# Kernel tuning notes

Measured on AMD Instinct MI355X. Metric: run time of the kernel, lower is better.

The kernel has to match this reference:

```python
import jax, jax.numpy as jnp
import numpy as np

E = 4
OUT_CH = 32
IN_CH = 32
KSIZE = 3
PAD = 1
TEMPERATURE = 30.0
HIDDEN = IN_CH // 4  # ratio=4


def _dyn_conv(x, w):
    """Per-sample conv. x: [B,C,H,W], w: [B,O,C,k,k] -> [B,O,H,W] (pad=1, stride=1)."""
    def one(xi, wi):
        return jax.lax.conv_general_dilated(
            xi[None], wi, window_strides=(1, 1), padding=[(PAD, PAD), (PAD, PAD)],
            dimension_numbers=('NCHW', 'OIHW', 'NCHW'))[0]
    return jax.vmap(one)(x, w)


def setup_inputs() -> dict:
    key = jax.random.key(0)
    ks = jax.random.split(key, 6)
    x = jax.random.normal(ks[0], (16, IN_CH, 256, 256), dtype=jnp.float32)
    # ControlModule 1x1 convs (bias=False) expressed as matrices
    w_c1 = jax.random.normal(ks[1], (HIDDEN, IN_CH), dtype=jnp.float32) * (2.0 / IN_CH) ** 0.5
    w_c2 = jax.random.normal(ks[2], (E * OUT_CH, HIDDEN), dtype=jnp.float32) * (2.0 / HIDDEN) ** 0.5
    weight1 = jax.random.normal(ks[3], (E, OUT_CH, IN_CH, KSIZE, KSIZE), dtype=jnp.float32)
    weight2 = jax.random.normal(ks[4], (E, OUT_CH, OUT_CH, KSIZE, KSIZE), dtype=jnp.float32)
    weight3 = jax.random.normal(ks[5], (E, OUT_CH, OUT_CH, KSIZE, KSIZE), dtype=jnp.float32)
    return {"x": x, "w_c1": w_c1, "w_c2": w_c2,
            "weight1": weight1, "weight2": weight2, "weight3": weight3}


def reference(x, w_c1, w_c2, weight1, weight2, weight3):
    B = x.shape[0]
    # ControlModule: global average pool -> 1x1 conv -> relu -> 1x1 conv -> softmax over E
    gap = x.mean(axis=(2, 3))                      # [B, C]
    h = jax.nn.relu(gap @ w_c1.T)                  # [B, hidden]
    coeff = (h @ w_c2.T).reshape(B, OUT_CH, E)     # [B, O, E]
    coeff = jax.nn.softmax(coeff / TEMPERATURE, axis=2)

    def assemble(w):  # w: [E, O, C, k, k] -> per-sample [B, O, C, k, k]
        flat = w.reshape(E, OUT_CH, -1)
        agg = jnp.einsum('boe,eoc->boc', coeff, flat)
        return agg.reshape(B, OUT_CH, *w.shape[2:])

    w1 = assemble(weight1)
    w2 = assemble(weight2)
    w3 = assemble(weight3)

    out = _dyn_conv(x, w1)
    out = _dyn_conv(out, w2)
    out = _dyn_conv(out, w3)
    return out
```

## Files before the change

kernel.cpp:

```cpp
#include <hip/hip_runtime.h>

typedef __attribute__((ext_vector_type(8))) short bf16x8;
typedef __attribute__((ext_vector_type(4))) float f32x4;

#define B_   16
#define HW_  256
#define HID_ 8
#define TEMP_ 30.0f

static __device__ inline unsigned short f2bf(float f) {
    unsigned u = __builtin_bit_cast(unsigned, f);
    u = (u + 0x7FFFu + ((u >> 16) & 1u)) >> 16;
    return (unsigned short)u;
}
static __device__ inline unsigned packbf(float a, float b) {
    return (unsigned)f2bf(a) | ((unsigned)f2bf(b) << 16);
}

__global__ __launch_bounds__(256) void gap_kernel(const float* __restrict__ x,
                                                  float* __restrict__ gap) {
    int blk = blockIdx.x;
    int bc = blk >> 2, q = blk & 3;
    const float4* p = (const float4*)(x + ((size_t)bc << 16)) + q * 4096;
    int t = threadIdx.x;
    float s = 0.f;
#pragma unroll
    for (int i = 0; i < 16; ++i) {
        float4 v = p[i * 256 + t];
        s += v.x + v.y + v.z + v.w;
    }
    __shared__ float red[256];
    red[t] = s;
    __syncthreads();
    for (int off = 128; off > 0; off >>= 1) {
        if (t < off) red[t] += red[t + off];
        __syncthreads();
    }
    if (t == 0) atomicAdd(&gap[bc], red[0] * (1.f / 65536.f));
}

__global__ __launch_bounds__(256) void assemble_kernel(
    const float* __restrict__ gap,
    const float* __restrict__ w_c1,
    const float* __restrict__ w_c2,
    const float* __restrict__ wt1,
    const float* __restrict__ wt2,
    const float* __restrict__ wt3,
    unsigned short* __restrict__ wo1,
    unsigned short* __restrict__ wo2,
    unsigned short* __restrict__ wo3)
{
    int b = blockIdx.x;
    int sel = blockIdx.y;
    int t = threadIdx.x;
    __shared__ float gap_s[32], h_s[8], logit_s[128], coeff_s[32][4];
    if (t < 32) gap_s[t] = gap[b * 32 + t];
    __syncthreads();
    if (t < HID_) {
        float a = 0.f;
        for (int c = 0; c < 32; ++c) a += gap_s[c] * w_c1[t * 32 + c];
        h_s[t] = a > 0.f ? a : 0.f;
    }
    __syncthreads();
    if (t < 128) {
        float a = 0.f;
        for (int k = 0; k < HID_; ++k) a += h_s[k] * w_c2[t * HID_ + k];
        logit_s[t] = a * (1.0f / TEMP_);
    }
    __syncthreads();
    if (t < 32) {
        float m = -1e30f;
        for (int e = 0; e < 4; ++e) m = fmaxf(m, logit_s[t * 4 + e]);
        float ex[4], sum = 0.f;
        for (int e = 0; e < 4; ++e) { ex[e] = expf(logit_s[t * 4 + e] - m); sum += ex[e]; }
        for (int e = 0; e < 4; ++e) coeff_s[t][e] = ex[e] / sum;
    }
    __syncthreads();

    const float* wt = sel == 0 ? wt1 : (sel == 1 ? wt2 : wt3);
    unsigned short* wo = sel == 0 ? wo1 : (sel == 1 ? wo2 : wo3);

    for (int idx = t; idx < 9216; idx += 256) {
        int d = idx >> 10;
        int o = (idx >> 5) & 31;
        int c = idx & 31;
        int j = c * 9 + d;
        float v = coeff_s[o][0] * wt[(0 * 32 + o) * 288 + j]
                + coeff_s[o][1] * wt[(1 * 32 + o) * 288 + j]
                + coeff_s[o][2] * wt[(2 * 32 + o) * 288 + j]
                + coeff_s[o][3] * wt[(3 * 32 + o) * 288 + j];
        wo[(size_t)b * 9216 + idx] = f2bf(v);
    }
}

template<int IN_F32, int OUT_F32>
__global__ __launch_bounds__(256) void conv3x3_mfma(
    const void* __restrict__ src,
    const unsigned short* __restrict__ wgt,
    void* __restrict__ dst)
{
    __shared__ uint4 lds[2448];
    int b  = blockIdx.z;
    int x0 = blockIdx.x * 32, y0 = blockIdx.y * 16;
    int t  = threadIdx.x;
    int l15 = t & 15;
    int kg  = (t >> 4) & 3;
    int wv  = t >> 6;

    bf16x8 wf[9][2];
    {
        const uint4* wp = (const uint4*)(wgt + (size_t)b * 9216);
#pragma unroll
        for (int d = 0; d < 9; ++d)
#pragma unroll
            for (int ob = 0; ob < 2; ++ob)
                wf[d][ob] = __builtin_bit_cast(bf16x8, wp[(d * 32 + ob * 16 + l15) * 4 + kg]);
    }

#pragma unroll
    for (int it = 0; it < 10; ++it) {
        int tau = it * 256 + t;
        if (tau < 2448) {
            int px = tau >> 2, cg = tau & 3;
            int yy = px / 34;
            int xx = px - yy * 34;
            int gy = y0 - 1 + yy, gx = x0 - 1 + xx;
            uint4 v = make_uint4(0u, 0u, 0u, 0u);
            if ((unsigned)gy < 256u && (unsigned)gx < 256u) {
                if (IN_F32) {
                    const float* sp = (const float*)src
                        + (((size_t)b * 32 + cg * 8) << 16) + (gy << 8) + gx;
                    float f0 = sp[0],         f1 = sp[1 << 16];
                    float f2 = sp[2 << 16],   f3 = sp[3 << 16];
                    float f4 = sp[4 << 16],   f5 = sp[5 << 16];
                    float f6 = sp[6 << 16],   f7 = sp[7 << 16];
                    v.x = packbf(f0, f1); v.y = packbf(f2, f3);
                    v.z = packbf(f4, f5); v.w = packbf(f6, f7);
                } else {
                    v = *((const uint4*)src
                          + (((size_t)b << 16) + (gy << 8) + gx) * 4 + cg);
                }
            }
            lds[tau] = v;
        }
    }
    __syncthreads();

    const bf16x8* lp = (const bf16x8*)lds;
#pragma unroll
    for (int r = 0; r < 4; ++r) {
        int yl = wv * 4 + r;
#pragma unroll
        for (int xt = 0; xt < 2; ++xt) {
            int base = (yl * 34 + xt * 16 + l15) * 4 + kg;
            f32x4 a0 = {0.f, 0.f, 0.f, 0.f};
            f32x4 a1 = {0.f, 0.f, 0.f, 0.f};
#pragma unroll
            for (int d = 0; d < 9; ++d) {
                bf16x8 bfr = lp[base + ((d / 3) * 34 + (d % 3)) * 4];
                a0 = __builtin_amdgcn_mfma_f32_16x16x32_bf16(wf[d][0], bfr, a0, 0, 0, 0);
                a1 = __builtin_amdgcn_mfma_f32_16x16x32_bf16(wf[d][1], bfr, a1, 0, 0, 0);
            }
            int gy = y0 + yl, gx = x0 + xt * 16 + l15;
            if (OUT_F32) {
                float* dp = (float*)dst + (((size_t)b * 32 + kg * 4) << 16) + (gy << 8) + gx;
#pragma unroll
                for (int r2 = 0; r2 < 4; ++r2) {
                    dp[(size_t)r2 << 16]        = a0[r2];
                    dp[(size_t)(r2 + 16) << 16] = a1[r2];
                }
            } else {
                unsigned short* dp = (unsigned short*)dst
                    + ((((size_t)b << 16) + (gy << 8) + gx) * 32) + kg * 4;
                uint2 p0, p1;
                p0.x = packbf(a0[0], a0[1]); p0.y = packbf(a0[2], a0[3]);
                p1.x = packbf(a1[0], a1[1]); p1.y = packbf(a1[2], a1[3]);
                *(uint2*)dp        = p0;
                *(uint2*)(dp + 16) = p1;
            }
        }
    }
}

extern "C" void kernel_launch(void* const* d_in, const int* in_sizes, int n_in,
                              void* d_out, int out_size, void* d_ws, size_t ws_size,
                              hipStream_t stream) {
    const float* x    = (const float*)d_in[0];
    const float* w_c1 = (const float*)d_in[1];
    const float* w_c2 = (const float*)d_in[2];
    const float* wt1  = (const float*)d_in[3];
    const float* wt2  = (const float*)d_in[4];
    const float* wt3  = (const float*)d_in[5];
    float* out = (float*)d_out;

    char* ws = (char*)d_ws;
    float* gap = (float*)ws;
    unsigned short* w1 = (unsigned short*)(ws + 2048);
    unsigned short* w2 = w1 + 147456;
    unsigned short* w3 = w2 + 147456;
    unsigned short* t1 = (unsigned short*)(ws + 983040);
    unsigned short* t2 = (unsigned short*)(ws + 983040 + 67108864);

    hipMemsetAsync(gap, 0, 2048, stream);
    gap_kernel<<<2048, 256, 0, stream>>>(x, gap);
    assemble_kernel<<<dim3(16, 3), 256, 0, stream>>>(gap, w_c1, w_c2,
                                                     wt1, wt2, wt3, w1, w2, w3);
    dim3 cg(8, 16, B_);
    conv3x3_mfma<1, 0><<<cg, 256, 0, stream>>>(x,  w1, t1);
    conv3x3_mfma<0, 0><<<cg, 256, 0, stream>>>(t1, w2, t2);
    conv3x3_mfma<0, 1><<<cg, 256, 0, stream>>>(t2, w3, out);
}
```

Measured before the change: 409.4 us.

## Fuse three dynamic convs into one halo-tiled kernel and fuse GAP with bf16 conversion

```diff
diff --git a/kernel.cpp b/kernel.cpp
--- a/kernel.cpp
+++ b/kernel.cpp
@@ -3,10 +3,8 @@
 typedef __attribute__((ext_vector_type(8))) short bf16x8;
 typedef __attribute__((ext_vector_type(4))) float f32x4;
 
-#define B_   16
-#define HW_  256
-#define HID_ 8
 #define TEMP_ 30.0f
+#define MFMA(A,B,C) __builtin_amdgcn_mfma_f32_16x16x32_bf16(A,B,C,0,0,0)
 
 static __device__ inline unsigned short f2bf(float f) {
     unsigned u = __builtin_bit_cast(unsigned, f);
@@ -16,27 +14,57 @@
 static __device__ inline unsigned packbf(float a, float b) {
     return (unsigned)f2bf(a) | ((unsigned)f2bf(b) << 16);
 }
-
-__global__ __launch_bounds__(256) void gap_kernel(const float* __restrict__ x,
-                                                  float* __restrict__ gap) {
-    int blk = blockIdx.x;
-    int bc = blk >> 2, q = blk & 3;
-    const float4* p = (const float4*)(x + ((size_t)bc << 16)) + q * 4096;
-    int t = threadIdx.x;
-    float s = 0.f;
-#pragma unroll
-    for (int i = 0; i < 16; ++i) {
-        float4 v = p[i * 256 + t];
-        s += v.x + v.y + v.z + v.w;
-    }
-    __shared__ float red[256];
-    red[t] = s;
-    __syncthreads();
-    for (int off = 128; off > 0; off >>= 1) {
-        if (t < off) red[t] += red[t + off];
-        __syncthreads();
-    }
-    if (t == 0) atomicAdd(&gap[bc], red[0] * (1.f / 65536.f));
+static __device__ inline bf16x8 bc16(uint4 v) { return __builtin_bit_cast(bf16x8, v); }
+
+__global__ __launch_bounds__(256) void gap_cvt_kernel(
+    const float* __restrict__ x, float* __restrict__ gap,
+    unsigned short* __restrict__ xbf)
+{
+    __shared__ unsigned short sm[32 * 4 * 258];
+    __shared__ float red[4][32];
+    int b = blockIdx.y, ys = blockIdx.x * 4;
+    int t = threadIdx.x, wv = t >> 6, ln = t & 63;
+
+    const float* xb = x + (((size_t)b * 32) << 16) + ((size_t)(ys + wv) << 8) + ln * 4;
+    float part[32];
+#pragma unroll
+    for (int c = 0; c < 32; ++c) {
+        float4 v = *(const float4*)(xb + ((size_t)c << 16));
+        part[c] = v.x + v.y + v.z + v.w;
+        unsigned* wp = (unsigned*)&sm[c * 1032 + wv * 258 + ln * 4];
+        wp[0] = packbf(v.x, v.y);
+        wp[1] = packbf(v.z, v.w);
+    }
+#pragma unroll
+    for (int c = 0; c < 32; ++c) {
+#pragma unroll
+        for (int off = 32; off; off >>= 1) part[c] += __shfl_xor(part[c], off);
+    }
+    if (ln == 0) {
+#pragma unroll
+        for (int c = 0; c < 32; ++c) red[wv][c] = part[c];
+    }
+    __syncthreads();
+    if (t < 32) {
+        float s = red[0][t] + red[1][t] + red[2][t] + red[3][t];
+        atomicAdd(&gap[b * 32 + t], s * (1.f / 65536.f));
+    }
+    uint4* outp = (uint4*)xbf;
+    int cg = wv;
+#pragma unroll
+    for (int it = 0; it < 16; ++it) {
+        int px = it * 64 + ln;
+        int y = px >> 8, xx = px & 255;
+        unsigned short h[8];
+#pragma unroll
+        for (int i = 0; i < 8; ++i) h[i] = sm[(cg * 8 + i) * 1032 + y * 258 + xx];
+        uint4 v;
+        v.x = (unsigned)h[0] | ((unsigned)h[1] << 16);
+        v.y = (unsigned)h[2] | ((unsigned)h[3] << 16);
+        v.z = (unsigned)h[4] | ((unsigned)h[5] << 16);
+        v.w = (unsigned)h[6] | ((unsigned)h[7] << 16);
+        outp[((((size_t)b << 16) + ((size_t)(ys + y) << 8) + xx) << 2) + cg] = v;
+    }
 }
 
 __global__ __launch_bounds__(256) void assemble_kernel(
@@ -56,7 +84,7 @@
     __shared__ float gap_s[32], h_s[8], logit_s[128], coeff_s[32][4];
     if (t < 32) gap_s[t] = gap[b * 32 + t];
     __syncthreads();
-    if (t < HID_) {
+    if (t < 8) {
         float a = 0.f;
         for (int c = 0; c < 32; ++c) a += gap_s[c] * w_c1[t * 32 + c];
         h_s[t] = a > 0.f ? a : 0.f;
@@ -64,7 +92,7 @@
     __syncthreads();
     if (t < 128) {
         float a = 0.f;
-        for (int k = 0; k < HID_; ++k) a += h_s[k] * w_c2[t * HID_ + k];
+        for (int k = 0; k < 8; ++k) a += h_s[k] * w_c2[t * 8 + k];
         logit_s[t] = a * (1.0f / TEMP_);
     }
     __syncthreads();
@@ -93,91 +121,123 @@
     }
 }
 
-template<int IN_F32, int OUT_F32>
-__global__ __launch_bounds__(256) void conv3x3_mfma(
-    const void* __restrict__ src,
-    const unsigned short* __restrict__ wgt,
-    void* __restrict__ dst)
+__global__ __launch_bounds__(512, 2) void fused_conv3(
+    const unsigned short* __restrict__ xbf,
+    const unsigned short* __restrict__ w1,
+    const unsigned short* __restrict__ w2,
+    const unsigned short* __restrict__ w3,
+    float* __restrict__ out)
 {
-    __shared__ uint4 lds[2448];
+    __shared__ uint4 lds[7192];
     int b  = blockIdx.z;
     int x0 = blockIdx.x * 32, y0 = blockIdx.y * 16;
     int t  = threadIdx.x;
-    int l15 = t & 15;
-    int kg  = (t >> 4) & 3;
-    int wv  = t >> 6;
-
-    bf16x8 wf[9][2];
-    {
-        const uint4* wp = (const uint4*)(wgt + (size_t)b * 9216);
-#pragma unroll
-        for (int d = 0; d < 9; ++d)
-#pragma unroll
-            for (int ob = 0; ob < 2; ++ob)
-                wf[d][ob] = __builtin_bit_cast(bf16x8, wp[(d * 32 + ob * 16 + l15) * 4 + kg]);
-    }
-
-#pragma unroll
-    for (int it = 0; it < 10; ++it) {
-        int tau = it * 256 + t;
-        if (tau < 2448) {
-            int px = tau >> 2, cg = tau & 3;
-            int yy = px / 34;
-            int xx = px - yy * 34;
-            int gy = y0 - 1 + yy, gx = x0 - 1 + xx;
+    int l15 = t & 15, kg = (t >> 4) & 3, wv = t >> 6;
+
+    const uint4* wp1 = (const uint4*)(w1 + (size_t)b * 9216);
+    const uint4* wp2 = (const uint4*)(w2 + (size_t)b * 9216);
+    const uint4* wp3 = (const uint4*)(w3 + (size_t)b * 9216);
+
+    bf16x8 wfA[9][2], wfB[9][2];
+#pragma unroll
+    for (int d = 0; d < 9; ++d) {
+        wfA[d][0] = bc16(wp1[(d * 32 + l15) * 4 + kg]);
+        wfA[d][1] = bc16(wp1[(d * 32 + 16 + l15) * 4 + kg]);
+    }
+
+    const unsigned short* xb = xbf + (((size_t)b) << 16) * 32;
+    for (int it = 0; it < 7; ++it) {
+        int tau = it * 512 + t;
+        if (tau < 3344) {
+            int y = tau / 152, rem = tau - y * 152;
+            int xx = rem >> 2, cg = rem & 3;
+            int gy = y0 - 3 + y, gx = x0 - 3 + xx;
             uint4 v = make_uint4(0u, 0u, 0u, 0u);
-            if ((unsigned)gy < 256u && (unsigned)gx < 256u) {
-                if (IN_F32) {
-                    const float* sp = (const float*)src
-                        + (((size_t)b * 32 + cg * 8) << 16) + (gy << 8) + gx;
-                    float f0 = sp[0],         f1 = sp[1 << 16];
-                    float f2 = sp[2 << 16],   f3 = sp[3 << 16];
-                    float f4 = sp[4 << 16],   f5 = sp[5 << 16];
-                    float f6 = sp[6 << 16],   f7 = sp[7 << 16];
-                    v.x = packbf(f0, f1); v.y = packbf(f2, f3);
-                    v.z = packbf(f4, f5); v.w = packbf(f6, f7);
-                } else {
-                    v = *((const uint4*)src
-                          + (((size_t)b << 16) + (gy << 8) + gx) * 4 + cg);
-                }
-            }
+            if ((unsigned)gy < 256u && (unsigned)gx < 256u)
+                v = *(const uint4*)(xb + ((((size_t)gy << 8) + gx) << 5) + (cg << 3));
             lds[tau] = v;
         }
     }
-    __syncthreads();
-
-    const bf16x8* lp = (const bf16x8*)lds;
-#pragma unroll
-    for (int r = 0; r < 4; ++r) {
-        int yl = wv * 4 + r;
-#pragma unroll
-        for (int xt = 0; xt < 2; ++xt) {
-            int base = (yl * 34 + xt * 16 + l15) * 4 + kg;
-            f32x4 a0 = {0.f, 0.f, 0.f, 0.f};
-            f32x4 a1 = {0.f, 0.f, 0.f, 0.f};
-#pragma unroll
-            for (int d = 0; d < 9; ++d) {
-                bf16x8 bfr = lp[base + ((d / 3) * 34 + (d % 3)) * 4];
-                a0 = __builtin_amdgcn_mfma_f32_16x16x32_bf16(wf[d][0], bfr, a0, 0, 0, 0);
-                a1 = __builtin_amdgcn_mfma_f32_16x16x32_bf16(wf[d][1], bfr, a1, 0, 0, 0);
-            }
-            int gy = y0 + yl, gx = x0 + xt * 16 + l15;
-            if (OUT_F32) {
-                float* dp = (float*)dst + (((size_t)b * 32 + kg * 4) << 16) + (gy << 8) + gx;
-#pragma unroll
-                for (int r2 = 0; r2 < 4; ++r2) {
-                    dp[(size_t)r2 << 16]        = a0[r2];
-                    dp[(size_t)(r2 + 16) << 16] = a1[r2];
-                }
-            } else {
-                unsigned short* dp = (unsigned short*)dst
-                    + ((((size_t)b << 16) + (gy << 8) + gx) * 32) + kg * 4;
-                uint2 p0, p1;
-                p0.x = packbf(a0[0], a0[1]); p0.y = packbf(a0[2], a0[3]);
-                p1.x = packbf(a1[0], a1[1]); p1.y = packbf(a1[2], a1[3]);
-                *(uint2*)dp        = p0;
-                *(uint2*)(dp + 16) = p1;
-            }
+#pragma unroll
+    for (int d = 0; d < 9; ++d) {
+        wfB[d][0] = bc16(wp2[(d * 32 + l15) * 4 + kg]);
+        wfB[d][1] = bc16(wp2[(d * 32 + 16 + l15) * 4 + kg]);
+    }
+    __syncthreads();
+
+    const bf16x8* LA = (const bf16x8*)lds;
+    const bf16x8* L1 = (const bf16x8*)(lds + 3344);
+    unsigned short* SA = (unsigned short*)lds;
+    unsigned short* S1 = (unsigned short*)(lds + 3344);
+
+    for (int i = wv; i < 60; i += 8) {
+        int row = i / 3, xt = i - row * 3;
+        int Xp = xt * 16 + l15;
+        int base = (row * 38 + Xp) * 4 + kg;
+        f32x4 a0 = {0.f,0.f,0.f,0.f}, a1 = {0.f,0.f,0.f,0.f};
+#pragma unroll
+        for (int d = 0; d < 9; ++d) {
+            bf16x8 bfr = LA[base + (d / 3) * 152 + (d % 3) * 4];
+            a0 = MFMA(wfA[d][0], bfr, a0);
+            a1 = MFMA(wfA[d][1], bfr, a1);
+        }
+        bool live = ((unsigned)(y0 - 2 + row) < 256u) && ((unsigned)(x0 - 2 + Xp) < 256u);
+        uint2 p0, p1;
+        p0.x = packbf(a0[0], a0[1]); p0.y = packbf(a0[2], a0[3]);
+        p1.x = packbf(a1[0], a1[1]); p1.y = packbf(a1[2], a1[3]);
+        if (!live) { p0.x = p0.y = p1.x = p1.y = 0u; }
+        unsigned short* dp = S1 + ((row * 48 + Xp) << 5);
+        *(uint2*)(dp + (kg << 2))      = p0;
+        *(uint2*)(dp + 16 + (kg << 2)) = p1;
+    }
+#pragma unroll
+    for (int d = 0; d < 9; ++d) {
+        wfA[d][0] = bc16(wp3[(d * 32 + l15) * 4 + kg]);
+        wfA[d][1] = bc16(wp3[(d * 32 + 16 + l15) * 4 + kg]);
+    }
+    __syncthreads();
+
+    for (int i = wv; i < 54; i += 8) {
+        int row = i / 3, xt = i - row * 3;
+        int Xp = xt * 16 + l15;
+        int base = (row * 48 + Xp) * 4 + kg;
+        f32x4 a0 = {0.f,0.f,0.f,0.f}, a1 = {0.f,0.f,0.f,0.f};
+#pragma unroll
+        for (int d = 0; d < 9; ++d) {
+            bf16x8 bfr = L1[base + (d / 3) * 192 + (d % 3) * 4];
+            a0 = MFMA(wfB[d][0], bfr, a0);
+            a1 = MFMA(wfB[d][1], bfr, a1);
+        }
+        if (Xp < 34) {
+            bool live = ((unsigned)(y0 - 1 + row) < 256u) && ((unsigned)(x0 - 1 + Xp) < 256u);
+            uint2 p0, p1;
+            p0.x = packbf(a0[0], a0[1]); p0.y = packbf(a0[2], a0[3]);
+            p1.x = packbf(a1[0], a1[1]); p1.y = packbf(a1[2], a1[3]);
+            if (!live) { p0.x = p0.y = p1.x = p1.y = 0u; }
+            unsigned short* dp = SA + ((row * 34 + Xp) << 5);
+            *(uint2*)(dp + (kg << 2))      = p0;
+            *(uint2*)(dp + 16 + (kg << 2)) = p1;
+        }
+    }
+    __syncthreads();
+
+    for (int i = wv; i < 32; i += 8) {
+        int row = i >> 1, xt = i & 1;
+        int Xp = xt * 16 + l15;
+        int base = (row * 34 + Xp) * 4 + kg;
+        f32x4 a0 = {0.f,0.f,0.f,0.f}, a1 = {0.f,0.f,0.f,0.f};
+#pragma unroll
+        for (int d = 0; d < 9; ++d) {
+            bf16x8 bfr = LA[base + (d / 3) * 136 + (d % 3) * 4];
+            a0 = MFMA(wfA[d][0], bfr, a0);
+            a1 = MFMA(wfA[d][1], bfr, a1);
+        }
+        int gy = y0 + row, gx = x0 + Xp;
+        float* dp = out + (((size_t)b * 32 + kg * 4) << 16) + ((size_t)gy << 8) + gx;
+#pragma unroll
+        for (int r2 = 0; r2 < 4; ++r2) {
+            dp[(size_t)r2 << 16]        = a0[r2];
+            dp[(size_t)(r2 + 16) << 16] = a1[r2];
         }
     }
 }
@@ -195,18 +255,14 @@
 
     char* ws = (char*)d_ws;
     float* gap = (float*)ws;
-    unsigned short* w1 = (unsigned short*)(ws + 2048);
-    unsigned short* w2 = w1 + 147456;
-    unsigned short* w3 = w2 + 147456;
-    unsigned short* t1 = (unsigned short*)(ws + 983040);
-    unsigned short* t2 = (unsigned short*)(ws + 983040 + 67108864);
+    unsigned short* w1 = (unsigned short*)(ws + 4096);
+    unsigned short* w2 = (unsigned short*)(ws + 4096 + 294912);
+    unsigned short* w3 = (unsigned short*)(ws + 4096 + 2 * 294912);
+    unsigned short* xbf = (unsigned short*)(ws + 1048576);
 
     hipMemsetAsync(gap, 0, 2048, stream);
-    gap_kernel<<<2048, 256, 0, stream>>>(x, gap);
+    gap_cvt_kernel<<<dim3(64, 16), 256, 0, stream>>>(x, gap, xbf);
     assemble_kernel<<<dim3(16, 3), 256, 0, stream>>>(gap, w_c1, w_c2,
                                                      wt1, wt2, wt3, w1, w2, w3);
-    dim3 cg(8, 16, B_);
-    conv3x3_mfma<1, 0><<<cg, 256, 0, stream>>>(x,  w1, t1);
-    conv3x3_mfma<0, 0><<<cg, 256, 0, stream>>>(t1, w2, t2);
-    conv3x3_mfma<0, 1><<<cg, 256, 0, stream>>>(t2, w3, out);
-}
+    fused_conv3<<<dim3(8, 16, 16), 512, 0, stream>>>(xbf, w1, w2, w3, out);
+}
```

Result: faster. 389.1 us (-5.0%).
